# Kernel optimization log

Hardware: AMD Instinct MI355X
Metric: run time of the kernel (lower is better)

The kernel has to match this reference:

```python
import jax, jax.numpy as jnp
import numpy as np

# Constants from the module's docstrings / vm_step / constants
VOCAB = 272
D_MODEL = 512
CODE_START = 256  # Token.CODE_START (first special after 256 byte tokens)
CODE_END = 257    # Token.CODE_END
MEM = 258         # Token.MEM
ADDR_KEY = 206    # _SetDim.ADDR_KEY (48 dims: 3 nibbles x 16 one-hot)
MEM_STORE = 455   # _SetDim.MEM_STORE
BYTES_PER_INSTR = 5
INSTR_WIDTH = 8


def setup_inputs() -> dict:
    key = jax.random.key(0)
    k1, k2 = jax.random.split(key)
    token_ids = jax.random.randint(k1, (32, 8192), 0, VOCAB)
    embed_table = jax.random.normal(k2, (VOCAB, D_MODEL), dtype=jnp.float32)
    return {"token_ids": token_ids, "embed_table": embed_table, "mem_history_end": 2048}


def reference(token_ids, embed_table, mem_history_end):
    B, S = token_ids.shape
    x = embed_table[token_ids]                     # [B, S, D] gather
    pos = jnp.arange(S)

    # ---- ADDR_KEY injection (vectorized replacement of the per-token loop) ----
    is_cs = token_ids == CODE_START
    is_ce = token_ids == CODE_END
    # most recent CODE_START position at or before i (-1 if none yet)
    cs = jax.lax.cummax(jnp.where(is_cs, pos[None, :], -1), axis=1)       # [B, S]
    # the python loop breaks the row at the FIRST CODE_END
    first_ce = jnp.min(jnp.where(is_ce, pos[None, :], S), axis=1, keepdims=True)  # [B, 1]
    is_byte = token_ids < 256
    mask = (cs >= 0) & (pos[None, :] < first_ce) & is_byte                # [B, S]

    seq_pos = jnp.maximum(pos[None, :] - cs - 1, 0)                       # >=0 where mask
    addr = (seq_pos // BYTES_PER_INSTR) * INSTR_WIDTH + seq_pos % BYTES_PER_INSTR
    lo = addr & 15
    hi = (addr >> 4) & 15
    top = (addr >> 8) & 15

    nib = jnp.arange(16)
    onehot48 = jnp.concatenate(
        [lo[..., None] == nib, hi[..., None] == nib, top[..., None] == nib], axis=-1
    )  # [B, S, 48] bool

    seg = x[..., ADDR_KEY:ADDR_KEY + 48]
    seg = jnp.where(mask[..., None] & onehot48, jnp.float32(1.0), seg)
    x = x.at[..., ADDR_KEY:ADDR_KEY + 48].set(seg)

    # ---- MEM_STORE injection on historical MEM markers ----
    mem_mask = (token_ids == MEM) & (pos[None, :] < mem_history_end)
    ch = jnp.where(mem_mask, jnp.float32(1.0), x[..., MEM_STORE])
    x = x.at[..., MEM_STORE].set(ch)
    return x
```

## Files before the change

kernel.cpp:

```cpp
#include <hip/hip_runtime.h>
#include <hip/hip_bf16.h>

#define B 32
#define S 8192
#define D 512
#define CODE_START 256
#define CODE_END 257
#define MEM_TOK 258
#define ADDR_KEY 206
#define MEM_STORE 455
#define CHUNK 512
#define NCH (S / CHUNK)

typedef float f32x4 __attribute__((ext_vector_type(4)));

__global__ __launch_bounds__(256) void nvm_carry(
    const int* __restrict__ tok, int* __restrict__ carry, int* __restrict__ mince) {
  const int c = blockIdx.x, b = blockIdx.y;
  const int tid = threadIdx.x;
  const int lane = tid & 63, wid = tid >> 6;
  const int p0 = c * CHUNK + 2 * tid;
  int2 tt = reinterpret_cast<const int2*>(tok + b * S + c * CHUNK)[tid];
  int vmax = max(tt.x == CODE_START ? p0 : -1, tt.y == CODE_START ? p0 + 1 : -1);
  int vmin = min(tt.x == CODE_END ? p0 : S, tt.y == CODE_END ? p0 + 1 : S);
  #pragma unroll
  for (int off = 32; off; off >>= 1) {
    vmax = max(vmax, __shfl_down(vmax, off, 64));
    vmin = min(vmin, __shfl_down(vmin, off, 64));
  }
  __shared__ int smax[4], smin[4];
  if (lane == 0) { smax[wid] = vmax; smin[wid] = vmin; }
  __syncthreads();
  if (tid == 0) {
    carry[b * NCH + c] = max(max(smax[0], smax[1]), max(smax[2], smax[3]));
    mince[b * NCH + c] = min(min(smin[0], smin[1]), min(smin[2], smin[3]));
  }
}

__device__ inline int make_pack(int tk, int cs, int p, int f, int mhe) {
  int pk = tk;
  if ((cs >= 0) && (p < f) && (tk < 256)) {
    int sp = p - cs - 1;
    if (sp < 0) sp = 0;
    int q = sp / 5;
    int r = sp - q * 5;
    int addr = q * 8 + r;
    pk |= (1 << 9) | ((addr & 15) << 12) | (((addr >> 4) & 15) << 16) |
          (((addr >> 8) & 15) << 20);
  }
  if (tk == MEM_TOK && p < mhe) pk |= (1 << 10);
  return pk;
}

__global__ __launch_bounds__(256) void nvm_main(
    const int* __restrict__ tok, const float* __restrict__ table,
    const int* __restrict__ carry, const int* __restrict__ mince,
    const int* __restrict__ mhe_p, float* __restrict__ out) {
  const int c = blockIdx.x, b = blockIdx.y;
  const int tid = threadIdx.x;
  const int lane = tid & 63, wid = tid >> 6;
  const int base = c * CHUNK;

  __shared__ int pack_sh[CHUNK];
  __shared__ int wt[4];

  int2 tt = reinterpret_cast<const int2*>(tok + b * S + base)[tid];
  const int p0 = base + 2 * tid;
  const int v0 = (tt.x == CODE_START) ? p0 : -1;
  const int v1 = (tt.y == CODE_START) ? p0 + 1 : -1;
  const int i1 = max(v0, v1);
  int incl = i1;
  #pragma unroll
  for (int off = 1; off < 64; off <<= 1) {
    int u = __shfl_up(incl, off, 64);
    if (lane >= off) incl = max(incl, u);
  }
  int ex = __shfl_up(incl, 1, 64);
  if (lane == 0) ex = -1;
  if (lane == 63) wt[wid] = incl;
  __syncthreads();
  int pre = -1;
  for (int w = 0; w < wid; ++w) pre = max(pre, wt[w]);
  for (int c2 = 0; c2 < c; ++c2) pre = max(pre, carry[b * NCH + c2]);
  ex = max(ex, pre);
  const int cs0 = max(ex, v0);
  const int cs1 = max(ex, i1);

  int f = S;
  #pragma unroll
  for (int c2 = 0; c2 < NCH; ++c2) f = min(f, mince[b * NCH + c2]);
  const int mhe = mhe_p[0];

  pack_sh[2 * tid] = make_pack(tt.x, cs0, p0, f, mhe);
  pack_sh[2 * tid + 1] = make_pack(tt.y, cs1, p0 + 1, f, mhe);
  __syncthreads();

  const int ln = tid & 127;
  const int half = tid >> 7;
  const int c0 = ln * 4;
  float* outb = out + (size_t)(b * S + base) * D;

  #pragma unroll 4
  for (int j = 0; j < CHUNK / 2; ++j) {
    const int i = 2 * j + half;
    const int p = pack_sh[i];
    const int tk = p & 511;
    f32x4 v = *reinterpret_cast<const f32x4*>(table + tk * D + c0);
    if (p & (1 << 9)) {
      const int ca = ADDR_KEY + ((p >> 12) & 15);
      const int cb = ADDR_KEY + 16 + ((p >> 16) & 15);
      const int cc = ADDR_KEY + 32 + ((p >> 20) & 15);
      #pragma unroll
      for (int u = 0; u < 4; ++u) {
        const int ch = c0 + u;
        if (ch == ca || ch == cb || ch == cc) v[u] = 1.0f;
      }
    }
    if ((p & (1 << 10)) && c0 == (MEM_STORE & ~3)) v[MEM_STORE & 3] = 1.0f;
    __builtin_nontemporal_store(v, reinterpret_cast<f32x4*>(outb + (size_t)i * D + c0));
  }
}

extern "C" void kernel_launch(void* const* d_in, const int* in_sizes, int n_in,
                              void* d_out, int out_size, void* d_ws, size_t ws_size,
                              hipStream_t stream) {
  const int* tok = (const int*)d_in[0];
  const float* table = (const float*)d_in[1];
  const int* mhe = (const int*)d_in[2];
  float* out = (float*)d_out;

  int* carry = (int*)d_ws;
  int* mince = carry + B * NCH;

  nvm_carry<<<dim3(NCH, B), 256, 0, stream>>>(tok, carry, mince);
  nvm_main<<<dim3(NCH, B), 256, 0, stream>>>(tok, table, carry, mince, mhe, out);
}
```

Measured before the change: 111.5 us.

## Fuse carry pass into main kernel with per-block full-row token scan

Removes the separate carry/min-CODE_END kernel and its workspace round trip. Each block now rescans the whole 8192-token row to compute the prior CODE_START max and the first CODE_END, then handles a 128-token sub-chunk. Blocks grow from 512 to 2048, which adds parallelism but makes the token row read redundantly by every block (served mostly from cache). The aim is to save a launch and the dependency between the two kernels.

Result: faster. 106.4 us (-4.5%).

```diff
diff --git a/kernel.cpp b/kernel.cpp
--- a/kernel.cpp
+++ b/kernel.cpp
@@ -9,33 +9,11 @@
 #define MEM_TOK 258
 #define ADDR_KEY 206
 #define MEM_STORE 455
-#define CHUNK 512
-#define NCH (S / CHUNK)
+#define SUB 128
+#define NSUB (S / SUB)
 
 typedef float f32x4 __attribute__((ext_vector_type(4)));
-
-__global__ __launch_bounds__(256) void nvm_carry(
-    const int* __restrict__ tok, int* __restrict__ carry, int* __restrict__ mince) {
-  const int c = blockIdx.x, b = blockIdx.y;
-  const int tid = threadIdx.x;
-  const int lane = tid & 63, wid = tid >> 6;
-  const int p0 = c * CHUNK + 2 * tid;
-  int2 tt = reinterpret_cast<const int2*>(tok + b * S + c * CHUNK)[tid];
-  int vmax = max(tt.x == CODE_START ? p0 : -1, tt.y == CODE_START ? p0 + 1 : -1);
-  int vmin = min(tt.x == CODE_END ? p0 : S, tt.y == CODE_END ? p0 + 1 : S);
-  #pragma unroll
-  for (int off = 32; off; off >>= 1) {
-    vmax = max(vmax, __shfl_down(vmax, off, 64));
-    vmin = min(vmin, __shfl_down(vmin, off, 64));
-  }
-  __shared__ int smax[4], smin[4];
-  if (lane == 0) { smax[wid] = vmax; smin[wid] = vmin; }
-  __syncthreads();
-  if (tid == 0) {
-    carry[b * NCH + c] = max(max(smax[0], smax[1]), max(smax[2], smax[3]));
-    mince[b * NCH + c] = min(min(smin[0], smin[1]), min(smin[2], smin[3]));
-  }
-}
+typedef int i32x4 __attribute__((ext_vector_type(4)));
 
 __device__ inline int make_pack(int tk, int cs, int p, int f, int mhe) {
   int pk = tk;
@@ -52,60 +30,73 @@
   return pk;
 }
 
-__global__ __launch_bounds__(256) void nvm_main(
+__global__ __launch_bounds__(256) void nvm_fused(
     const int* __restrict__ tok, const float* __restrict__ table,
-    const int* __restrict__ carry, const int* __restrict__ mince,
     const int* __restrict__ mhe_p, float* __restrict__ out) {
-  const int c = blockIdx.x, b = blockIdx.y;
+  const int c = blockIdx.x;
+  const int b = blockIdx.y;
   const int tid = threadIdx.x;
   const int lane = tid & 63, wid = tid >> 6;
-  const int base = c * CHUNK;
+  const int base = c * SUB;
+  const int* row = tok + b * S;
 
-  __shared__ int pack_sh[CHUNK];
-  __shared__ int wt[4];
+  __shared__ int red_max[4], red_min[4], wt[2];
+  __shared__ int pack_sh[SUB];
 
-  int2 tt = reinterpret_cast<const int2*>(tok + b * S + base)[tid];
-  const int p0 = base + 2 * tid;
-  const int v0 = (tt.x == CODE_START) ? p0 : -1;
-  const int v1 = (tt.y == CODE_START) ? p0 + 1 : -1;
-  const int i1 = max(v0, v1);
-  int incl = i1;
+  int vmax = -1, vmin = S;
+  #pragma unroll
+  for (int k = 0; k < 8; ++k) {
+    const i32x4 q = reinterpret_cast<const i32x4*>(row)[tid + 256 * k];
+    const int p = 4 * (tid + 256 * k);
+    #pragma unroll
+    for (int e = 0; e < 4; ++e) {
+      const int t = q[e], pp = p + e;
+      if (t == CODE_START && pp < base) vmax = max(vmax, pp);
+      if (t == CODE_END) vmin = min(vmin, pp);
+    }
+  }
+  #pragma unroll
+  for (int off = 32; off; off >>= 1) {
+    vmax = max(vmax, __shfl_down(vmax, off, 64));
+    vmin = min(vmin, __shfl_down(vmin, off, 64));
+  }
+  if (lane == 0) { red_max[wid] = vmax; red_min[wid] = vmin; }
+
+  int myTok = 0, v = -1;
+  if (tid < SUB) {
+    myTok = row[base + tid];
+    v = (myTok == CODE_START) ? (base + tid) : -1;
+  }
+  int incl = v;
   #pragma unroll
   for (int off = 1; off < 64; off <<= 1) {
-    int u = __shfl_up(incl, off, 64);
+    const int u = __shfl_up(incl, off, 64);
     if (lane >= off) incl = max(incl, u);
   }
-  int ex = __shfl_up(incl, 1, 64);
-  if (lane == 0) ex = -1;
-  if (lane == 63) wt[wid] = incl;
+  if (tid < SUB && lane == 63) wt[wid] = incl;
   __syncthreads();
-  int pre = -1;
-  for (int w = 0; w < wid; ++w) pre = max(pre, wt[w]);
-  for (int c2 = 0; c2 < c; ++c2) pre = max(pre, carry[b * NCH + c2]);
-  ex = max(ex, pre);
-  const int cs0 = max(ex, v0);
-  const int cs1 = max(ex, i1);
 
-  int f = S;
-  #pragma unroll
-  for (int c2 = 0; c2 < NCH; ++c2) f = min(f, mince[b * NCH + c2]);
+  const int pre = max(max(red_max[0], red_max[1]), max(red_max[2], red_max[3]));
+  const int fce = min(min(red_min[0], red_min[1]), min(red_min[2], red_min[3]));
   const int mhe = mhe_p[0];
 
-  pack_sh[2 * tid] = make_pack(tt.x, cs0, p0, f, mhe);
-  pack_sh[2 * tid + 1] = make_pack(tt.y, cs1, p0 + 1, f, mhe);
+  if (tid < SUB) {
+    const int ex = (wid == 1) ? wt[0] : -1;
+    const int cs = max(max(incl, ex), pre);
+    pack_sh[tid] = make_pack(myTok, cs, base + tid, fce, mhe);
+  }
   __syncthreads();
 
-  const int ln = tid & 127;
-  const int half = tid >> 7;
+  const int ln = tid & 127, half = tid >> 7;
   const int c0 = ln * 4;
   float* outb = out + (size_t)(b * S + base) * D;
 
   #pragma unroll 4
-  for (int j = 0; j < CHUNK / 2; ++j) {
+  for (int j = 0; j < SUB / 2; ++j) {
     const int i = 2 * j + half;
     const int p = pack_sh[i];
     const int tk = p & 511;
-    f32x4 v = *reinterpret_cast<const f32x4*>(table + tk * D + c0);
+    f32x4 v4 = *reinterpret_cast<const f32x4*>(table + tk * D + c0);
     if (p & (1 << 9)) {
       const int ca = ADDR_KEY + ((p >> 12) & 15);
       const int cb = ADDR_KEY + 16 + ((p >> 16) & 15);
@@ -113,11 +104,11 @@
       #pragma unroll
       for (int u = 0; u < 4; ++u) {
         const int ch = c0 + u;
-        if (ch == ca || ch == cb || ch == cc) v[u] = 1.0f;
+        if (ch == ca || ch == cb || ch == cc) v4[u] = 1.0f;
       }
     }
-    if ((p & (1 << 10)) && c0 == (MEM_STORE & ~3)) v[MEM_STORE & 3] = 1.0f;
-    __builtin_nontemporal_store(v, reinterpret_cast<f32x4*>(outb + (size_t)i * D + c0));
+    if ((p & (1 << 10)) && c0 == (MEM_STORE & ~3)) v4[MEM_STORE & 3] = 1.0f;
+    __builtin_nontemporal_store(v4, reinterpret_cast<f32x4*>(outb + (size_t)i * D + c0));
   }
 }
 
@@ -129,9 +120,5 @@
   const int* mhe = (const int*)d_in[2];
   float* out = (float*)d_out;
 
-  int* carry = (int*)d_ws;
-  int* mince = carry + B * NCH;
-
-  nvm_carry<<<dim3(NCH, B), 256, 0, stream>>>(tok, carry, mince);
-  nvm_main<<<dim3(NCH, B), 256, 0, stream>>>(tok, table, carry, mince, mhe, out);
+  nvm_fused<<<dim3(NSUB, B), 256, 0, stream>>>(tok, table, mhe, out);
 }
```
